# Performance work log

Measured on AMD Instinct MI355X. Metric: run time of the kernel, lower is better.

Reference implementation:

```python
import jax, jax.numpy as jnp
import numpy as np

BOUNDING_PERC = 0.05

def setup_inputs() -> dict:
    key = jax.random.key(0)
    ks = jax.random.split(key, 8)
    b, nfaces, ncells, nb, in_dim, ksz = 4, 1_000_000, 500_000, 500_000, 4, 9
    kernel = jax.random.normal(ks[0], (b, nfaces, in_dim), dtype=jnp.float32)
    source = jax.random.normal(ks[1], (b, nfaces, 3, 3), dtype=jnp.float32)
    ucenters = jax.random.normal(ks[2], (b, ncells), dtype=jnp.float32)
    W = jax.random.normal(ks[3], (in_dim, ksz), dtype=jnp.float32)
    bias = jax.random.normal(ks[4], (ksz,), dtype=jnp.float32)
    positions = jnp.arange(nb, dtype=jnp.int32)  # unique boundary-face ids
    owners = jax.random.randint(ks[5], (nb,), 0, ncells, dtype=jnp.int32)
    neighbours = jax.random.randint(ks[6], (nb,), 0, ncells, dtype=jnp.int32)
    return {"kernel": kernel, "source": source, "ucenters": ucenters,
            "W": W, "bias": bias, "positions": positions,
            "owners": owners, "neighbours": neighbours}

def reference(kernel, source, ucenters, W, bias, positions, owners, neighbours):
    # constraint layer: affine map to per-face stencil coefficients [b, nfaces, ksz]
    coefficients = jnp.einsum('bxi,is->bxs', kernel, W) + bias
    b, nfaces = source.shape[0], source.shape[1]
    patches = source.reshape(b, nfaces, -1)          # [b, nfaces, ksz]
    ufaces = jnp.einsum('bxs,bxs->bx', coefficients, patches)  # [b, nfaces]
    # --- bounding on boundary faces ---
    ufaces_b = ufaces[:, positions]                   # [b, nb]
    owner = ucenters[:, owners]                       # [b, nb]
    neighbour = ucenters[:, neighbours]               # [b, nb]
    side_max = jnp.maximum(owner, neighbour)
    side_min = jnp.minimum(owner, neighbour)
    flux_cd = 0.5 * (owner + neighbour)
    upwind = jnp.where(flux_cd >= 0.0, owner, neighbour)
    upper_lim = side_max + BOUNDING_PERC * jnp.abs(side_max)
    lower_lim = side_min - BOUNDING_PERC * jnp.abs(side_min)
    valid = (ufaces_b >= lower_lim) & (ufaces_b <= upper_lim)
    ufaces_bounded = jnp.where(valid, ufaces_b, upwind)
    # scatter bounded values back into the full face array
    return ufaces.at[:, positions].set(ufaces_bounded)
```

## Files before the change

kernel.cpp:

```cpp
#include <hip/hip_runtime.h>

#define BOUNDING_PERC 0.05f

__global__ __launch_bounds__(256) void ufaces_kernel(
    const float4* __restrict__ k4,
    const float4* __restrict__ s4,
    const float*  __restrict__ W,
    const float*  __restrict__ bias,
    float*        __restrict__ out)
{
    __shared__ float s_src[2304];
    const int tid       = threadIdx.x;
    const int base_face = blockIdx.x << 8;

    {
        const float4* src_blk = s4 + ((size_t)base_face * 9) / 4;
        float4* sm4 = reinterpret_cast<float4*>(s_src);
        sm4[tid]       = src_blk[tid];
        sm4[tid + 256] = src_blk[tid + 256];
        if (tid < 64) sm4[tid + 512] = src_blk[tid + 512];
    }

    float Wr[4][9];
#pragma unroll
    for (int i = 0; i < 4; ++i)
#pragma unroll
        for (int s = 0; s < 9; ++s)
            Wr[i][s] = W[i * 9 + s];
    float br[9];
#pragma unroll
    for (int s = 0; s < 9; ++s) br[s] = bias[s];

    const float4 kv = k4[base_face + tid];

    __syncthreads();

    const float* S = &s_src[tid * 9];
    float acc = 0.0f;
#pragma unroll
    for (int s = 0; s < 9; ++s) {
        float c = br[s];
        c = fmaf(kv.x, Wr[0][s], c);
        c = fmaf(kv.y, Wr[1][s], c);
        c = fmaf(kv.z, Wr[2][s], c);
        c = fmaf(kv.w, Wr[3][s], c);
        acc = fmaf(c, S[s], acc);
    }
    out[base_face + tid] = acc;
}

__global__ __launch_bounds__(256) void bound_kernel(
    const float* __restrict__ uc,
    const int*   __restrict__ pos,
    const int*   __restrict__ own,
    const int*   __restrict__ nei,
    float*       __restrict__ out,
    int nb, int nfaces, int ncells, int nbatch)
{
    int idx = blockIdx.x * blockDim.x + threadIdx.x;
    if (idx >= nbatch * nb) return;
    int j  = idx % nb;
    int bb = idx / nb;

    int p = pos[j];
    float uf = out[bb * nfaces + p];
    float o  = uc[bb * ncells + own[j]];
    float n  = uc[bb * ncells + nei[j]];

    float smax = fmaxf(o, n);
    float smin = fminf(o, n);
    float flux = 0.5f * (o + n);
    float up   = (flux >= 0.0f) ? o : n;
    float hi   = smax + BOUNDING_PERC * fabsf(smax);
    float lo   = smin - BOUNDING_PERC * fabsf(smin);
    bool valid = (uf >= lo) && (uf <= hi);
    out[bb * nfaces + p] = valid ? uf : up;
}

extern "C" void kernel_launch(void* const* d_in, const int* in_sizes, int n_in,
                              void* d_out, int out_size, void* d_ws, size_t ws_size,
                              hipStream_t stream)
{
    const float* kernel_in  = (const float*)d_in[0];
    const float* source     = (const float*)d_in[1];
    const float* ucenters   = (const float*)d_in[2];
    const float* W          = (const float*)d_in[3];
    const float* bias       = (const float*)d_in[4];
    const int*   positions  = (const int*)d_in[5];
    const int*   owners     = (const int*)d_in[6];
    const int*   neighbours = (const int*)d_in[7];
    float*       out        = (float*)d_out;

    const int b      = 4;
    const int in_dim = 4;
    const int nfaces = in_sizes[0] / (b * in_dim);
    const int ncells = in_sizes[2] / b;
    const int nb     = in_sizes[5];

    const int total_faces = b * nfaces;

    {
        dim3 block(256);
        dim3 grid(total_faces / 256);
        ufaces_kernel<<<grid, block, 0, stream>>>(
            (const float4*)kernel_in, (const float4*)source, W, bias, out);
    }

    {
        int total = b * nb;
        dim3 block(256);
        dim3 grid((total + 255) / 256);
        bound_kernel<<<grid, block, 0, stream>>>(
            ucenters, positions, owners, neighbours, out,
            nb, nfaces, ncells, b);
    }
}
```

Baseline: 60.82 us.

## Fuse bounding into face kernel via inverse position map

Builds an inverse map from face index to boundary index in workspace (memset to -1, then scatter), so the main face kernel can apply the bounding logic inline and write each output once. This removes the second pass that re-read and re-wrote the output at scattered positions. In exchange it adds a memset, a small scatter kernel, a coalesced read of the inverse map per face, and a branch with gathers of ucenters inside the main kernel. It falls back to the old two-kernel path if the workspace is too small.

```diff
diff --git a/kernel.cpp b/kernel.cpp
--- a/kernel.cpp
+++ b/kernel.cpp
@@ -2,19 +2,34 @@
 
 #define BOUNDING_PERC 0.05f
 
-__global__ __launch_bounds__(256) void ufaces_kernel(
+__global__ __launch_bounds__(256) void scatter_inv_kernel(
+    const int* __restrict__ pos, int* __restrict__ inv, int nb)
+{
+    int j = blockIdx.x * blockDim.x + threadIdx.x;
+    if (j < nb) inv[pos[j]] = j;
+}
+
+__global__ __launch_bounds__(256) void fused_kernel(
     const float4* __restrict__ k4,
     const float4* __restrict__ s4,
     const float*  __restrict__ W,
     const float*  __restrict__ bias,
-    float*        __restrict__ out)
+    const int*    __restrict__ inv,
+    const float*  __restrict__ uc,
+    const int*    __restrict__ own,
+    const int*    __restrict__ nei,
+    float*        __restrict__ out,
+    int nfaces, int ncells)
 {
     __shared__ float s_src[2304];
-    const int tid       = threadIdx.x;
-    const int base_face = blockIdx.x << 8;
+    const int tid   = threadIdx.x;
+    const int gbase = blockIdx.x << 8;
+    const int g     = gbase + tid;
+    const int bb    = g / nfaces;
+    const int f     = g - bb * nfaces;
 
     {
-        const float4* src_blk = s4 + ((size_t)base_face * 9) / 4;
+        const float4* src_blk = s4 + ((size_t)gbase * 9) / 4;
         float4* sm4 = reinterpret_cast<float4*>(s_src);
         sm4[tid]       = src_blk[tid];
         sm4[tid + 256] = src_blk[tid + 256];
@@ -31,10 +46,64 @@
 #pragma unroll
     for (int s = 0; s < 9; ++s) br[s] = bias[s];
 
-    const float4 kv = k4[base_face + tid];
+    const float4 kv = k4[g];
+    const int j = inv[f];
 
     __syncthreads();
 
+    const float* S = &s_src[tid * 9];
+    float acc = 0.0f;
+#pragma unroll
+    for (int s = 0; s < 9; ++s) {
+        float c = br[s];
+        c = fmaf(kv.x, Wr[0][s], c);
+        c = fmaf(kv.y, Wr[1][s], c);
+        c = fmaf(kv.z, Wr[2][s], c);
+        c = fmaf(kv.w, Wr[3][s], c);
+        acc = fmaf(c, S[s], acc);
+    }
+
+    float res = acc;
+    if (j >= 0) {
+        float o = uc[bb * ncells + own[j]];
+        float n = uc[bb * ncells + nei[j]];
+        float smax = fmaxf(o, n);
+        float smin = fminf(o, n);
+        float flux = 0.5f * (o + n);
+        float up   = (flux >= 0.0f) ? o : n;
+        float hi   = smax + BOUNDING_PERC * fabsf(smax);
+        float lo   = smin - BOUNDING_PERC * fabsf(smin);
+        bool valid = (acc >= lo) && (acc <= hi);
+        res = valid ? acc : up;
+    }
+    out[g] = res;
+}
+
+__global__ __launch_bounds__(256) void ufaces_kernel(
+    const float4* __restrict__ k4, const float4* __restrict__ s4,
+    const float* __restrict__ W, const float* __restrict__ bias,
+    float* __restrict__ out)
+{
+    __shared__ float s_src[2304];
+    const int tid = threadIdx.x;
+    const int base_face = blockIdx.x << 8;
+    {
+        const float4* src_blk = s4 + ((size_t)base_face * 9) / 4;
+        float4* sm4 = reinterpret_cast<float4*>(s_src);
+        sm4[tid]       = src_blk[tid];
+        sm4[tid + 256] = src_blk[tid + 256];
+        if (tid < 64) sm4[tid + 512] = src_blk[tid + 512];
+    }
+    float Wr[4][9];
+#pragma unroll
+    for (int i = 0; i < 4; ++i)
+#pragma unroll
+        for (int s = 0; s < 9; ++s) Wr[i][s] = W[i * 9 + s];
+    float br[9];
+#pragma unroll
+    for (int s = 0; s < 9; ++s) br[s] = bias[s];
+    const float4 kv = k4[base_face + tid];
+    __syncthreads();
     const float* S = &s_src[tid * 9];
     float acc = 0.0f;
 #pragma unroll
@@ -50,23 +119,18 @@
 }
 
 __global__ __launch_bounds__(256) void bound_kernel(
-    const float* __restrict__ uc,
-    const int*   __restrict__ pos,
-    const int*   __restrict__ own,
-    const int*   __restrict__ nei,
-    float*       __restrict__ out,
-    int nb, int nfaces, int ncells, int nbatch)
+    const float* __restrict__ uc, const int* __restrict__ pos,
+    const int* __restrict__ own, const int* __restrict__ nei,
+    float* __restrict__ out, int nb, int nfaces, int ncells, int nbatch)
 {
     int idx = blockIdx.x * blockDim.x + threadIdx.x;
     if (idx >= nbatch * nb) return;
     int j  = idx % nb;
     int bb = idx / nb;
-
     int p = pos[j];
     float uf = out[bb * nfaces + p];
     float o  = uc[bb * ncells + own[j]];
     float n  = uc[bb * ncells + nei[j]];
-
     float smax = fmaxf(o, n);
     float smin = fminf(o, n);
     float flux = 0.5f * (o + n);
@@ -96,22 +160,20 @@
     const int nfaces = in_sizes[0] / (b * in_dim);
     const int ncells = in_sizes[2] / b;
     const int nb     = in_sizes[5];
-
     const int total_faces = b * nfaces;
 
-    {
-        dim3 block(256);
-        dim3 grid(total_faces / 256);
-        ufaces_kernel<<<grid, block, 0, stream>>>(
+    if (ws_size >= (size_t)nfaces * sizeof(int)) {
+        int* inv = (int*)d_ws;
+        hipMemsetAsync(inv, 0xFF, (size_t)nfaces * sizeof(int), stream);
+        scatter_inv_kernel<<<(nb + 255) / 256, 256, 0, stream>>>(positions, inv, nb);
+        fused_kernel<<<total_faces / 256, 256, 0, stream>>>(
+            (const float4*)kernel_in, (const float4*)source, W, bias,
+            inv, ucenters, owners, neighbours, out, nfaces, ncells);
+    } else {
+        ufaces_kernel<<<total_faces / 256, 256, 0, stream>>>(
             (const float4*)kernel_in, (const float4*)source, W, bias, out);
-    }
-
-    {
         int total = b * nb;
-        dim3 block(256);
-        dim3 grid((total + 255) / 256);
-        bound_kernel<<<grid, block, 0, stream>>>(
-            ucenters, positions, owners, neighbours, out,
-            nb, nfaces, ncells, b);
+        bound_kernel<<<(total + 255) / 256, 256, 0, stream>>>(
+            ucenters, positions, owners, neighbours, out, nb, nfaces, ncells, b);
     }
 }
```

Result: no change. 61.94 us (+1.8%).

## Fuse face evaluation and boundary bounding via per-face owner/neighbour map

Applied to the files above, without the earlier changes.

Builds a per-face owner/neighbour table in workspace, with a memset to mark non-boundary faces and a scatter kernel to fill boundary entries. A single fused kernel then computes each face value and applies the bounding in registers, so the read-modify-write pass over out done by a second kernel is gone. Each wave now handles 128 faces using per-wave shared memory, with no block barrier, and uses nontemporal loads and stores. The cost is an extra memset and scatter over an 8-byte-per-face table on every call, and the fast path depends on the workspace being large enough.

```diff
diff --git a/kernel.cpp b/kernel.cpp
--- a/kernel.cpp
+++ b/kernel.cpp
@@ -2,17 +2,135 @@
 
 #define BOUNDING_PERC 0.05f
 
+typedef float  f32x4 __attribute__((ext_vector_type(4)));
+typedef float  f32x2 __attribute__((ext_vector_type(2)));
+
+__global__ __launch_bounds__(256) void scatter_on_kernel(
+    const int* __restrict__ pos, const int* __restrict__ own,
+    const int* __restrict__ nei, int2* __restrict__ own_nei, int nb)
+{
+    int j = blockIdx.x * blockDim.x + threadIdx.x;
+    if (j < nb) {
+        int2 v; v.x = own[j]; v.y = nei[j];
+        own_nei[pos[j]] = v;
+    }
+}
+
+__global__ __launch_bounds__(256) void fused_kernel(
+    const f32x4* __restrict__ k4,
+    const f32x4* __restrict__ s4,
+    const float* __restrict__ W,
+    const float* __restrict__ bias,
+    const int2*  __restrict__ own_nei,
+    const float* __restrict__ uc,
+    float*       __restrict__ out,
+    int nfaces, int ncells, int total_faces)
+{
+    __shared__ float smem[4 * 1152];
+    const int tid  = threadIdx.x;
+    const int wv   = tid >> 6;
+    const int lane = tid & 63;
+    float* mysm = smem + wv * 1152;
+
+    const int gw = (blockIdx.x << 9) + (wv << 7);
+    if (gw >= total_faces) return;
+
+    const f32x4* sb = s4 + ((size_t)gw * 9) / 4;
+    f32x4 a0 = __builtin_nontemporal_load(sb + lane);
+    f32x4 a1 = __builtin_nontemporal_load(sb + lane + 64);
+    f32x4 a2 = __builtin_nontemporal_load(sb + lane + 128);
+    f32x4 a3 = __builtin_nontemporal_load(sb + lane + 192);
+    const f32x2* sb2 = reinterpret_cast<const f32x2*>(sb);
+    f32x2 a4 = __builtin_nontemporal_load(sb2 + 512 + lane);
+    f32x4 kv0 = __builtin_nontemporal_load(k4 + gw + lane);
+    f32x4 kv1 = __builtin_nontemporal_load(k4 + gw + 64 + lane);
+
+    const int g0 = gw + lane;
+    const int g1 = gw + 64 + lane;
+    const int bb0 = g0 / nfaces;  const int f0 = g0 - bb0 * nfaces;
+    const int bb1 = g1 / nfaces;  const int f1 = g1 - bb1 * nfaces;
+    const int2 on0 = own_nei[f0];
+    const int2 on1 = own_nei[f1];
+
+    f32x4* m4 = reinterpret_cast<f32x4*>(mysm);
+    m4[lane]       = a0;
+    m4[lane + 64]  = a1;
+    m4[lane + 128] = a2;
+    m4[lane + 192] = a3;
+    f32x2* m2 = reinterpret_cast<f32x2*>(mysm);
+    m2[512 + lane] = a4;
+
+    float o0 = 0.0f, n0 = 0.0f, o1 = 0.0f, n1 = 0.0f;
+    const bool lim0 = (on0.x >= 0);
+    const bool lim1 = (on1.x >= 0);
+    if (lim0) {
+        const float* ucb = uc + (size_t)bb0 * ncells;
+        o0 = ucb[on0.x]; n0 = ucb[on0.y];
+    }
+    if (lim1) {
+        const float* ucb = uc + (size_t)bb1 * ncells;
+        o1 = ucb[on1.x]; n1 = ucb[on1.y];
+    }
+
+    float Wr[4][9];
+#pragma unroll
+    for (int i = 0; i < 4; ++i)
+#pragma unroll
+        for (int s = 0; s < 9; ++s)
+            Wr[i][s] = W[i * 9 + s];
+    float br[9];
+#pragma unroll
+    for (int s = 0; s < 9; ++s) br[s] = bias[s];
+
+    const float* S0 = mysm + lane * 9;
+    const float* S1 = mysm + (64 + lane) * 9;
+    float acc0 = 0.0f, acc1 = 0.0f;
+#pragma unroll
+    for (int s = 0; s < 9; ++s) {
+        float c0 = br[s];
+        c0 = fmaf(kv0.x, Wr[0][s], c0);
+        c0 = fmaf(kv0.y, Wr[1][s], c0);
+        c0 = fmaf(kv0.z, Wr[2][s], c0);
+        c0 = fmaf(kv0.w, Wr[3][s], c0);
+        acc0 = fmaf(c0, S0[s], acc0);
+        float c1 = br[s];
+        c1 = fmaf(kv1.x, Wr[0][s], c1);
+        c1 = fmaf(kv1.y, Wr[1][s], c1);
+        c1 = fmaf(kv1.z, Wr[2][s], c1);
+        c1 = fmaf(kv1.w, Wr[3][s], c1);
+        acc1 = fmaf(c1, S1[s], acc1);
+    }
+
+    float res0 = acc0;
+    if (lim0) {
+        float smax = fmaxf(o0, n0), smin = fminf(o0, n0);
+        float flux = 0.5f * (o0 + n0);
+        float up   = (flux >= 0.0f) ? o0 : n0;
+        float hi   = smax + BOUNDING_PERC * fabsf(smax);
+        float lo   = smin - BOUNDING_PERC * fabsf(smin);
+        res0 = (acc0 >= lo && acc0 <= hi) ? acc0 : up;
+    }
+    float res1 = acc1;
+    if (lim1) {
+        float smax = fmaxf(o1, n1), smin = fminf(o1, n1);
+        float flux = 0.5f * (o1 + n1);
+        float up   = (flux >= 0.0f) ? o1 : n1;
+        float hi   = smax + BOUNDING_PERC * fabsf(smax);
+        float lo   = smin - BOUNDING_PERC * fabsf(smin);
+        res1 = (acc1 >= lo && acc1 <= hi) ? acc1 : up;
+    }
+    __builtin_nontemporal_store(res0, out + g0);
+    __builtin_nontemporal_store(res1, out + g1);
+}
+
 __global__ __launch_bounds__(256) void ufaces_kernel(
-    const float4* __restrict__ k4,
-    const float4* __restrict__ s4,
-    const float*  __restrict__ W,
-    const float*  __restrict__ bias,
-    float*        __restrict__ out)
+    const float4* __restrict__ k4, const float4* __restrict__ s4,
+    const float* __restrict__ W, const float* __restrict__ bias,
+    float* __restrict__ out)
 {
     __shared__ float s_src[2304];
-    const int tid       = threadIdx.x;
+    const int tid = threadIdx.x;
     const int base_face = blockIdx.x << 8;
-
     {
         const float4* src_blk = s4 + ((size_t)base_face * 9) / 4;
         float4* sm4 = reinterpret_cast<float4*>(s_src);
@@ -20,21 +138,16 @@
         sm4[tid + 256] = src_blk[tid + 256];
         if (tid < 64) sm4[tid + 512] = src_blk[tid + 512];
     }
-
     float Wr[4][9];
 #pragma unroll
     for (int i = 0; i < 4; ++i)
 #pragma unroll
-        for (int s = 0; s < 9; ++s)
-            Wr[i][s] = W[i * 9 + s];
+        for (int s = 0; s < 9; ++s) Wr[i][s] = W[i * 9 + s];
     float br[9];
 #pragma unroll
     for (int s = 0; s < 9; ++s) br[s] = bias[s];
-
     const float4 kv = k4[base_face + tid];
-
     __syncthreads();
-
     const float* S = &s_src[tid * 9];
     float acc = 0.0f;
 #pragma unroll
@@ -50,25 +163,19 @@
 }
 
 __global__ __launch_bounds__(256) void bound_kernel(
-    const float* __restrict__ uc,
-    const int*   __restrict__ pos,
-    const int*   __restrict__ own,
-    const int*   __restrict__ nei,
-    float*       __restrict__ out,
-    int nb, int nfaces, int ncells, int nbatch)
+    const float* __restrict__ uc, const int* __restrict__ pos,
+    const int* __restrict__ own, const int* __restrict__ nei,
+    float* __restrict__ out, int nb, int nfaces, int ncells, int nbatch)
 {
     int idx = blockIdx.x * blockDim.x + threadIdx.x;
     if (idx >= nbatch * nb) return;
     int j  = idx % nb;
     int bb = idx / nb;
-
     int p = pos[j];
     float uf = out[bb * nfaces + p];
     float o  = uc[bb * ncells + own[j]];
     float n  = uc[bb * ncells + nei[j]];
-
-    float smax = fmaxf(o, n);
-    float smin = fminf(o, n);
+    float smax = fmaxf(o, n), smin = fminf(o, n);
     float flux = 0.5f * (o + n);
     float up   = (flux >= 0.0f) ? o : n;
     float hi   = smax + BOUNDING_PERC * fabsf(smax);
@@ -96,22 +203,24 @@
     const int nfaces = in_sizes[0] / (b * in_dim);
     const int ncells = in_sizes[2] / b;
     const int nb     = in_sizes[5];
-
     const int total_faces = b * nfaces;
 
-    {
-        dim3 block(256);
-        dim3 grid(total_faces / 256);
-        ufaces_kernel<<<grid, block, 0, stream>>>(
+    if (ws_size >= (size_t)nfaces * sizeof(int2)) {
+        int2* own_nei = (int2*)d_ws;
+        hipMemsetAsync(own_nei, 0xFF, (size_t)nfaces * sizeof(int2), stream);
+        scatter_on_kernel<<<(nb + 255) / 256, 256, 0, stream>>>(
+            positions, owners, neighbours, own_nei, nb);
+
+        const int faces_per_block = 512;
+        const int grid = (total_faces + faces_per_block - 1) / faces_per_block;
+        fused_kernel<<<grid, 256, 0, stream>>>(
+            (const f32x4*)kernel_in, (const f32x4*)source, W, bias,
+            (const int2*)own_nei, ucenters, out, nfaces, ncells, total_faces);
+    } else {
+        ufaces_kernel<<<total_faces / 256, 256, 0, stream>>>(
             (const float4*)kernel_in, (const float4*)source, W, bias, out);
-    }
-
-    {
         int total = b * nb;
-        dim3 block(256);
-        dim3 grid((total + 255) / 256);
-        bound_kernel<<<grid, block, 0, stream>>>(
-            ucenters, positions, owners, neighbours, out,
-            nb, nfaces, ncells, b);
-    }
-}
+        bound_kernel<<<(total + 255) / 256, 256, 0, stream>>>(
+            ucenters, positions, owners, neighbours, out, nb, nfaces, ncells, b);
+    }
+}
```

New measurement: 69.31 us. 1.14x slower.
